# Kernel tuning notes

Hardware: AMD Instinct MI355X
Metric: run time of the kernel (lower is better)

The kernel has to match this reference:

```python
import jax, jax.numpy as jnp
import numpy as np

B, S, E, H, L = 2, 2048, 1024, 16, 64


def setup_inputs() -> dict:
    key = jax.random.key(0)
    ks = jax.random.split(key, 9)
    x = jax.random.normal(ks[0], (B, S, E), dtype=jnp.float32)
    # causal mask: 1 where attention allowed, 0 where blocked (mask==0 -> -inf)
    mask = jnp.tril(jnp.ones((1, S, S), dtype=jnp.int32))
    std = 0.02
    # per-head Linear weights stacked over heads; torch Linear stores W as [out, in]
    Wq = jax.random.normal(ks[1], (H, L, E), dtype=jnp.float32) * std
    Wk = jax.random.normal(ks[2], (H, L, E), dtype=jnp.float32) * std
    Wv = jax.random.normal(ks[3], (H, L, E), dtype=jnp.float32) * std
    bq = jax.random.normal(ks[4], (H, L), dtype=jnp.float32) * std
    bk = jax.random.normal(ks[5], (H, L), dtype=jnp.float32) * std
    bv = jax.random.normal(ks[6], (H, L), dtype=jnp.float32) * std
    Wo = jax.random.normal(ks[7], (E, H * L), dtype=jnp.float32) * std
    bo = jax.random.normal(ks[8], (E,), dtype=jnp.float32) * std
    return {"x": x, "mask": mask, "Wq": Wq, "bq": bq, "Wk": Wk, "bk": bk,
            "Wv": Wv, "bv": bv, "Wo": Wo, "bo": bo}


def reference(x, mask, Wq, bq, Wk, bk, Wv, bv, Wo, bo):
    # Q/K/V for all heads at once: [B, H, S, L]
    Q = jnp.einsum('bse,hle->bhsl', x, Wq) + bq[None, :, None, :]
    K = jnp.einsum('bse,hle->bhsl', x, Wk) + bk[None, :, None, :]
    V = jnp.einsum('bse,hle->bhsl', x, Wv) + bv[None, :, None, :]
    scale = jnp.sqrt(jnp.asarray(L, dtype=Q.dtype))
    scores = jnp.einsum('bhsl,bhtl->bhst', Q, K) / scale  # [B,H,S,S]
    scores = jnp.where(mask[:, None, :, :] == 0, -jnp.inf, scores)
    P = jax.nn.softmax(scores, axis=-1)
    O = jnp.einsum('bhst,bhtl->bhsl', P, V)  # [B,H,S,L]
    # concat heads along last dim (head order matches torch concat)
    z = jnp.transpose(O, (0, 2, 1, 3)).reshape(O.shape[0], O.shape[2], -1)
    return jnp.einsum('bsk,ek->bse', z, Wo) + bo
```

## Files before the change

kernel.cpp:

```cpp
#include <hip/hip_runtime.h>
#include <math.h>

typedef unsigned short US;
typedef __attribute__((ext_vector_type(8))) __bf16 bf16x8;
typedef __attribute__((ext_vector_type(4))) float f32x4;
typedef __attribute__((ext_vector_type(4))) unsigned short us4;

#define MFMA16(a, b, c) __builtin_amdgcn_mfma_f32_16x16x32_bf16(a, b, c, 0, 0, 0)

__device__ __forceinline__ US f2bf(float f) {
  union { float f; unsigned u; } v; v.f = f;
  unsigned r = v.u + 0x7fffu + ((v.u >> 16) & 1u);
  return (US)(r >> 16);
}
__device__ __forceinline__ float bf2f(US u) {
  union { unsigned u; float f; } v; v.u = ((unsigned)u) << 16; return v.f;
}

__device__ __forceinline__ void gload16(const void* g, void* l) {
  __builtin_amdgcn_global_load_lds(
      (const __attribute__((address_space(1))) unsigned int*)g,
      (__attribute__((address_space(3))) unsigned int*)l, 16, 0, 0);
}

__global__ __launch_bounds__(256) void convert_k(
    const float* __restrict__ x, const float* __restrict__ Wq,
    const float* __restrict__ Wk, const float* __restrict__ Wv,
    const float* __restrict__ Wo,
    US* __restrict__ xb, US* __restrict__ wqkv, US* __restrict__ wob) {
  long i = (long)blockIdx.x * blockDim.x + threadIdx.x;
  long e4 = i * 4;
  if (e4 >= 8388608L) return;
  const float* src; US* dst;
  if (e4 < 4194304L) { src = x + e4; dst = xb + e4; }
  else if (e4 < 7340032L) {
    long off = e4 - 4194304L;
    dst = wqkv + off;
    src = (off < 1048576L) ? Wq + off
        : (off < 2097152L ? Wk + (off - 1048576L) : Wv + (off - 2097152L));
  } else {
    long off = e4 - 7340032L;
    src = Wo + off; dst = wob + off;
  }
  float4 v = *(const float4*)src;
  us4 o; o.x = f2bf(v.x); o.y = f2bf(v.y); o.z = f2bf(v.z); o.w = f2bf(v.w);
  *(us4*)dst = o;
}

template <int MODE>
__global__ __launch_bounds__(256) void gemm128(
    const US* __restrict__ A, const US* __restrict__ BT,
    int K, int lda, int ldb, int N,
    const float* __restrict__ b0, const float* __restrict__ b1,
    const float* __restrict__ b2,
    US* __restrict__ oQ, US* __restrict__ oK, US* __restrict__ oV,
    float* __restrict__ oF) {
  __shared__ __align__(16) US As[128 * 32];
  __shared__ __align__(16) US Bs[128 * 32];
  const int tid = threadIdx.x, lane = tid & 63;
  const int w = tid >> 6, wr = w >> 1, wc = w & 1;
  const int m0 = blockIdx.x * 128, n0 = blockIdx.y * 128;
  f32x4 acc[4][4] = {};
  const int r0 = tid >> 2, c0 = (tid & 3) * 8;

  for (int kt = 0; kt < K; kt += 32) {
    gload16(A + (size_t)(m0 + r0) * lda + kt + c0, As + tid * 8);
    gload16(A + (size_t)(m0 + r0 + 64) * lda + kt + c0, As + (tid + 256) * 8);
    gload16(BT + (size_t)(n0 + r0) * ldb + kt + c0, Bs + tid * 8);
    gload16(BT + (size_t)(n0 + r0 + 64) * ldb + kt + c0, Bs + (tid + 256) * 8);
    __syncthreads();
    bf16x8 af[4], bfm[4];
#pragma unroll
    for (int i = 0; i < 4; ++i)
      af[i] = *(const bf16x8*)(As + (wr * 64 + i * 16 + (lane & 15)) * 32 + (lane >> 4) * 8);
#pragma unroll
    for (int j = 0; j < 4; ++j)
      bfm[j] = *(const bf16x8*)(Bs + (wc * 64 + j * 16 + (lane & 15)) * 32 + (lane >> 4) * 8);
#pragma unroll
    for (int i = 0; i < 4; ++i)
#pragma unroll
      for (int j = 0; j < 4; ++j)
        acc[i][j] = MFMA16(af[i], bfm[j], acc[i][j]);
    __syncthreads();
  }

#pragma unroll
  for (int i = 0; i < 4; ++i) {
#pragma unroll
    for (int j = 0; j < 4; ++j) {
#pragma unroll
      for (int r = 0; r < 4; ++r) {
        int m = m0 + wr * 64 + i * 16 + (lane >> 4) * 4 + r;
        int n = n0 + wc * 64 + j * 16 + (lane & 15);
        float v = acc[i][j][r];
        if (MODE == 0) {
          int bb = m >> 11, s = m & 2047;
          int sec = n >> 10, idx = n & 1023;
          int h = idx >> 6, l = idx & 63;
          size_t bhsl = (((size_t)bb * 16 + h) * 2048 + s) * 64 + l;
          if (sec == 0)      oQ[bhsl] = f2bf((v + b0[idx]) * 0.125f);
          else if (sec == 1) oK[bhsl] = f2bf(v + b1[idx]);
          else oV[(((size_t)bb * 16 + h) * 64 + l) * 2048 + s] = f2bf(v + b2[idx]);
        } else {
          oF[(size_t)m * N + n] = v + b0[n];
        }
      }
    }
  }
}

__global__ __launch_bounds__(256) void attn_k(
    const US* __restrict__ Qb, const US* __restrict__ Kb,
    const US* __restrict__ Vtb, US* __restrict__ opart,
    float2* __restrict__ mlpart) {
  __shared__ __align__(16) US Ks[64 * 64];
  __shared__ __align__(16) US Vs[64 * 64];
  __shared__ __align__(16) US Ps[4][16 * 72];
  const int tid = threadIdx.x, lane = tid & 63, w = tid >> 6;
  const int slot = blockIdx.x >> 6;
  const int qt = 31 - slot;
  const int bh = (blockIdx.x & 63) >> 1;
  const int half = blockIdx.x & 1;
  const int h0 = (qt + 2) >> 1;
  const int kstart = half ? h0 : 0;
  const int kend = half ? (qt + 1) : h0;
  const size_t pslot = (size_t)(bh * 32 + qt) * 2 + half;

  if (kstart >= kend) {
    US* op = opart + pslot * 4096;
    us4 z; z.x = 0; z.y = 0; z.z = 0; z.w = 0;
#pragma unroll
    for (int j = 0; j < 4; ++j) *(us4*)(op + tid * 16 + j * 4) = z;
    if ((lane >> 4) == 0)
      mlpart[pslot * 64 + w * 16 + lane] = make_float2(-INFINITY, 0.f);
    return;
  }

  const US* Qp = Qb + ((size_t)bh * 2048 + qt * 64) * 64;
  const char* Kbase = (const char*)(Kb + (size_t)bh * 2048 * 64);
  const char* Vbase = (const char*)(Vtb + (size_t)bh * 64 * 2048);

  const int row0 = tid >> 3, col16 = (tid & 7) * 16;
  const int row1 = row0 + 32;
  const int soff0 = (row0 * 128 + col16) ^ ((row0 & 7) << 4);
  const int soff1 = soff0 + 32 * 128;

  bf16x8 aq[2];
  {
    int qrow = w * 16 + (lane & 15);
#pragma unroll
    for (int kk = 0; kk < 2; ++kk)
      aq[kk] = *(const bf16x8*)(Qp + qrow * 64 + kk * 32 + (lane >> 4) * 8);
  }
  f32x4 o[4] = {};
  float m = -INFINITY, l = 0.f;

  int4 rk0, rk1, rv0, rv1;
#define LOADT(KT)                                                              \
  do {                                                                         \
    rk0 = *(const int4*)(Kbase + ((size_t)((KT)*64 + row0)) * 128 + col16);    \
    rk1 = *(const int4*)(Kbase + ((size_t)((KT)*64 + row1)) * 128 + col16);    \
    rv0 = *(const int4*)(Vbase + (size_t)row0 * 4096 + (KT)*128 + col16);      \
    rv1 = *(const int4*)(Vbase + (size_t)row1 * 4096 + (KT)*128 + col16);      \
  } while (0)
#define WRITET()                                                               \
  do {                                                                         \
    *(int4*)((char*)Ks + soff0) = rk0;                                         \
    *(int4*)((char*)Ks + soff1) = rk1;                                         \
    *(int4*)((char*)Vs + soff0) = rv0;                                         \
    *(int4*)((char*)Vs + soff1) = rv1;                                         \
  } while (0)

  LOADT(kstart);
  WRITET();
  __syncthreads();

  for (int kt = kstart; kt < kend; ++kt) {
    if (kt + 1 < kend) LOADT(kt + 1);

    f32x4 sc[4];
    __builtin_amdgcn_s_setprio(1);
#pragma unroll
    for (int nt = 0; nt < 4; ++nt) {
      f32x4 s = {0.f, 0.f, 0.f, 0.f};
#pragma unroll
      for (int kk = 0; kk < 2; ++kk) {
        int rr = nt * 16 + (lane & 15);
        int off = rr * 128 + kk * 64 + (lane >> 4) * 16;
        off ^= (rr & 7) << 4;
        bf16x8 bkf = *(const bf16x8*)((const char*)Ks + off);
        s = MFMA16(bkf, aq[kk], s);
      }
      sc[nt] = s;
    }
    __builtin_amdgcn_s_setprio(0);

    if (kt == qt) {
      int q_in = w * 16 + (lane & 15);
#pragma unroll
      for (int nt = 0; nt < 4; ++nt)
#pragma unroll
        for (int r = 0; r < 4; ++r) {
          int kv_in = nt * 16 + (lane >> 4) * 4 + r;
          if (kv_in > q_in) sc[nt][r] = -INFINITY;
        }
    }

    {
      float m01 = fmaxf(fmaxf(sc[0][0], sc[0][1]), fmaxf(sc[0][2], sc[0][3]));
      float m23 = fmaxf(fmaxf(sc[1][0], sc[1][1]), fmaxf(sc[1][2], sc[1][3]));
      float m45 = fmaxf(fmaxf(sc[2][0], sc[2][1]), fmaxf(sc[2][2], sc[2][3]));
      float m67 = fmaxf(fmaxf(sc[3][0], sc[3][1]), fmaxf(sc[3][2], sc[3][3]));
      float mx = fmaxf(fmaxf(m01, m23), fmaxf(m45, m67));
      mx = fmaxf(mx, __shfl_xor(mx, 16));
      mx = fmaxf(mx, __shfl_xor(mx, 32));
      float mnew = fmaxf(m, mx);
      float scale = __expf(m - mnew);
      m = mnew;
      float s0 = 0.f, s1 = 0.f, s2 = 0.f, s3 = 0.f;
#pragma unroll
      for (int nt = 0; nt < 4; ++nt) {
        float p0 = __expf(sc[nt][0] - m);
        float p1 = __expf(sc[nt][1] - m);
        float p2 = __expf(sc[nt][2] - m);
        float p3 = __expf(sc[nt][3] - m);
        sc[nt][0] = p0; sc[nt][1] = p1; sc[nt][2] = p2; sc[nt][3] = p3;
        s0 += p0; s1 += p1; s2 += p2; s3 += p3;
      }
      float ssum = (s0 + s1) + (s2 + s3);
      ssum += __shfl_xor(ssum, 16);
      ssum += __shfl_xor(ssum, 32);
      l = l * scale + ssum;
#pragma unroll
      for (int r = 0; r < 4; ++r) {
        float sr = __shfl(scale, ((lane >> 4) << 2) + r, 64);
        o[0][r] *= sr; o[1][r] *= sr; o[2][r] *= sr; o[3][r] *= sr;
      }
    }

    US* pp = &Ps[w][0];
    const int pbase = (lane & 15) * 72 + (lane >> 4) * 4;
#pragma unroll
    for (int nt = 0; nt < 4; ++nt) {
      us4 w4;
      w4.x = f2bf(sc[nt][0]); w4.y = f2bf(sc[nt][1]);
      w4.z = f2bf(sc[nt][2]); w4.w = f2bf(sc[nt][3]);
      *(us4*)(pp + pbase + nt * 16) = w4;
    }

    __builtin_amdgcn_s_setprio(1);
#pragma unroll
    for (int kk = 0; kk < 2; ++kk) {
      bf16x8 pa = *(const bf16x8*)(pp + (lane & 15) * 72 + kk * 32 + (lane >> 4) * 8);
#pragma unroll
      for (int nt = 0; nt < 4; ++nt) {
        int rr = nt * 16 + (lane & 15);
        int off = rr * 128 + kk * 64 + (lane >> 4) * 16;
        off ^= (rr & 7) << 4;
        bf16x8 bvf = *(const bf16x8*)((const char*)Vs + off);
        o[nt] = MFMA16(pa, bvf, o[nt]);
      }
    }
    __builtin_amdgcn_s_setprio(0);

    __syncthreads();
    if (kt + 1 < kend) {
      WRITET();
      __syncthreads();
    }
  }
#undef LOADT
#undef WRITET

  US* op = opart + pslot * 4096;
#pragma unroll
  for (int r = 0; r < 4; ++r) {
    int row = w * 16 + (lane >> 4) * 4 + r;
#pragma unroll
    for (int nt = 0; nt < 4; ++nt) {
      int d = nt * 16 + (lane & 15);
      op[row * 64 + d] = f2bf(o[nt][r]);
    }
  }
  if ((lane >> 4) == 0)
    mlpart[pslot * 64 + w * 16 + lane] = make_float2(m, l);
}

__global__ __launch_bounds__(256) void merge_k(
    const US* __restrict__ opart, const float2* __restrict__ mlpart,
    US* __restrict__ zb) {
  const int t = blockIdx.x;
  const int bh = t >> 5, qt = t & 31;
  const int b = bh >> 4, h = bh & 15;
  const int row = threadIdx.x >> 2;
  const int dg = (threadIdx.x & 3) * 16;
  const US* o1 = opart + ((size_t)t * 2 + 0) * 4096 + row * 64 + dg;
  const US* o2 = opart + ((size_t)t * 2 + 1) * 4096 + row * 64 + dg;
  float2 ml1 = mlpart[(t * 2 + 0) * 64 + row];
  float2 ml2 = mlpart[(t * 2 + 1) * 64 + row];
  float mm = fmaxf(ml1.x, ml2.x);
  float w1 = __expf(ml1.x - mm), w2 = __expf(ml2.x - mm);
  float li = 1.0f / (ml1.y * w1 + ml2.y * w2);
  w1 *= li; w2 *= li;
  int s = qt * 64 + row;
  US* dst = zb + ((size_t)b * 2048 + s) * 1024 + h * 64 + dg;
#pragma unroll
  for (int j = 0; j < 4; ++j) {
    us4 a = *(const us4*)(o1 + j * 4);
    us4 c = *(const us4*)(o2 + j * 4);
    us4 r;
    r.x = f2bf(bf2f(a.x) * w1 + bf2f(c.x) * w2);
    r.y = f2bf(bf2f(a.y) * w1 + bf2f(c.y) * w2);
    r.z = f2bf(bf2f(a.z) * w1 + bf2f(c.z) * w2);
    r.w = f2bf(bf2f(a.w) * w1 + bf2f(c.w) * w2);
    *(us4*)(dst + j * 4) = r;
  }
}

extern "C" void kernel_launch(void* const* d_in, const int* in_sizes, int n_in,
                              void* d_out, int out_size, void* d_ws, size_t ws_size,
                              hipStream_t stream) {
  (void)in_sizes; (void)n_in; (void)out_size; (void)ws_size;
  const float* x  = (const float*)d_in[0];
  const float* Wq = (const float*)d_in[2];
  const float* bq = (const float*)d_in[3];
  const float* Wk = (const float*)d_in[4];
  const float* bk = (const float*)d_in[5];
  const float* Wv = (const float*)d_in[6];
  const float* bv = (const float*)d_in[7];
  const float* Wo = (const float*)d_in[8];
  const float* bo = (const float*)d_in[9];
  char* ws = (char*)d_ws;
  US* xb     = (US*)(ws);
  float2* ml = (float2*)(ws);
  US* zb     = (US*)(ws + 1048576);
  US* wqkv   = (US*)(ws + 8388608);
  US* wob    = (US*)(ws + 14680064);
  US* Qb     = (US*)(ws + 16777216);
  US* Kb     = (US*)(ws + 25165824);
  US* Vtb    = (US*)(ws + 33554432);
  US* opart  = (US*)d_out;
  float* out = (float*)d_out;

  convert_k<<<dim3(8192), dim3(256), 0, stream>>>(x, Wq, Wk, Wv, Wo, xb, wqkv, wob);
  gemm128<0><<<dim3(32, 24), dim3(256), 0, stream>>>(
      xb, wqkv, 1024, 1024, 1024, 3072, bq, bk, bv, Qb, Kb, Vtb, (float*)nullptr);
  attn_k<<<dim3(2048), dim3(256), 0, stream>>>(Qb, Kb, Vtb, opart, ml);
  merge_k<<<dim3(1024), dim3(256), 0, stream>>>(opart, ml, zb);
  gemm128<1><<<dim3(32, 8), dim3(256), 0, stream>>>(
      zb, wob, 1024, 1024, 1024, 1024, bo, (const float*)nullptr, (const float*)nullptr,
      (US*)nullptr, (US*)nullptr, (US*)nullptr, out);
}
```

Before: 140.4 us.

## Deepen GEMM K-step to 64 and switch softmax to exp2 with log2e-folded Q scale

The GEMM kernel now loads two 32-wide K slices per iteration into a doubled shared buffer, which halves the number of barrier pairs per tile. The cost is more LDS per block, which may lower occupancy. Separately, the log2(e) factor is folded into the Q scaling (0.125 becomes 0.18033688), so the attention and merge kernels can use exp2f instead of __expf and skip a multiply per exponential. This keeps the softmax mathematically equivalent up to rounding.

```diff
diff --git a/kernel.cpp b/kernel.cpp
--- a/kernel.cpp
+++ b/kernel.cpp
@@ -55,32 +55,42 @@
     const float* __restrict__ b2,
     US* __restrict__ oQ, US* __restrict__ oK, US* __restrict__ oV,
     float* __restrict__ oF) {
-  __shared__ __align__(16) US As[128 * 32];
-  __shared__ __align__(16) US Bs[128 * 32];
+  __shared__ __align__(16) US As[2][128 * 32];
+  __shared__ __align__(16) US Bs[2][128 * 32];
   const int tid = threadIdx.x, lane = tid & 63;
   const int w = tid >> 6, wr = w >> 1, wc = w & 1;
   const int m0 = blockIdx.x * 128, n0 = blockIdx.y * 128;
   f32x4 acc[4][4] = {};
   const int r0 = tid >> 2, c0 = (tid & 3) * 8;
 
-  for (int kt = 0; kt < K; kt += 32) {
-    gload16(A + (size_t)(m0 + r0) * lda + kt + c0, As + tid * 8);
-    gload16(A + (size_t)(m0 + r0 + 64) * lda + kt + c0, As + (tid + 256) * 8);
-    gload16(BT + (size_t)(n0 + r0) * ldb + kt + c0, Bs + tid * 8);
-    gload16(BT + (size_t)(n0 + r0 + 64) * ldb + kt + c0, Bs + (tid + 256) * 8);
+  for (int kt = 0; kt < K; kt += 64) {
+#pragma unroll
+    for (int h = 0; h < 2; ++h) {
+      gload16(A + (size_t)(m0 + r0) * lda + kt + h * 32 + c0, As[h] + tid * 8);
+      gload16(A + (size_t)(m0 + r0 + 64) * lda + kt + h * 32 + c0,
+              As[h] + (tid + 256) * 8);
+      gload16(BT + (size_t)(n0 + r0) * ldb + kt + h * 32 + c0, Bs[h] + tid * 8);
+      gload16(BT + (size_t)(n0 + r0 + 64) * ldb + kt + h * 32 + c0,
+              Bs[h] + (tid + 256) * 8);
+    }
     __syncthreads();
-    bf16x8 af[4], bfm[4];
-#pragma unroll
-    for (int i = 0; i < 4; ++i)
-      af[i] = *(const bf16x8*)(As + (wr * 64 + i * 16 + (lane & 15)) * 32 + (lane >> 4) * 8);
-#pragma unroll
-    for (int j = 0; j < 4; ++j)
-      bfm[j] = *(const bf16x8*)(Bs + (wc * 64 + j * 16 + (lane & 15)) * 32 + (lane >> 4) * 8);
-#pragma unroll
-    for (int i = 0; i < 4; ++i)
+#pragma unroll
+    for (int h = 0; h < 2; ++h) {
+      bf16x8 af[4], bfm[4];
+#pragma unroll
+      for (int i = 0; i < 4; ++i)
+        af[i] = *(const bf16x8*)(As[h] + (wr * 64 + i * 16 + (lane & 15)) * 32 +
+                                 (lane >> 4) * 8);
 #pragma unroll
       for (int j = 0; j < 4; ++j)
-        acc[i][j] = MFMA16(af[i], bfm[j], acc[i][j]);
+        bfm[j] = *(const bf16x8*)(Bs[h] + (wc * 64 + j * 16 + (lane & 15)) * 32 +
+                                  (lane >> 4) * 8);
+#pragma unroll
+      for (int i = 0; i < 4; ++i)
+#pragma unroll
+        for (int j = 0; j < 4; ++j)
+          acc[i][j] = MFMA16(af[i], bfm[j], acc[i][j]);
+    }
     __syncthreads();
   }
 
@@ -98,7 +108,7 @@
           int sec = n >> 10, idx = n & 1023;
           int h = idx >> 6, l = idx & 63;
           size_t bhsl = (((size_t)bb * 16 + h) * 2048 + s) * 64 + l;
-          if (sec == 0)      oQ[bhsl] = f2bf((v + b0[idx]) * 0.125f);
+          if (sec == 0)      oQ[bhsl] = f2bf((v + b0[idx]) * 0.18033688f);
           else if (sec == 1) oK[bhsl] = f2bf(v + b1[idx]);
           else oV[(((size_t)bb * 16 + h) * 64 + l) * 2048 + s] = f2bf(v + b2[idx]);
         } else {
@@ -215,15 +225,15 @@
       mx = fmaxf(mx, __shfl_xor(mx, 16));
       mx = fmaxf(mx, __shfl_xor(mx, 32));
       float mnew = fmaxf(m, mx);
-      float scale = __expf(m - mnew);
+      float scale = exp2f(m - mnew);
       m = mnew;
       float s0 = 0.f, s1 = 0.f, s2 = 0.f, s3 = 0.f;
 #pragma unroll
       for (int nt = 0; nt < 4; ++nt) {
-        float p0 = __expf(sc[nt][0] - m);
-        float p1 = __expf(sc[nt][1] - m);
-        float p2 = __expf(sc[nt][2] - m);
-        float p3 = __expf(sc[nt][3] - m);
+        float p0 = exp2f(sc[nt][0] - m);
+        float p1 = exp2f(sc[nt][1] - m);
+        float p2 = exp2f(sc[nt][2] - m);
+        float p3 = exp2f(sc[nt][3] - m);
         sc[nt][0] = p0; sc[nt][1] = p1; sc[nt][2] = p2; sc[nt][3] = p3;
         s0 += p0; s1 += p1; s2 += p2; s3 += p3;
       }
@@ -299,7 +309,7 @@
   float2 ml1 = mlpart[(t * 2 + 0) * 64 + row];
   float2 ml2 = mlpart[(t * 2 + 1) * 64 + row];
   float mm = fmaxf(ml1.x, ml2.x);
-  float w1 = __expf(ml1.x - mm), w2 = __expf(ml2.x - mm);
+  float w1 = exp2f(ml1.x - mm), w2 = exp2f(ml2.x - mm);
   float li = 1.0f / (ml1.y * w1 + ml2.y * w2);
   w1 *= li; w2 *= li;
   int s = qt * 64 + row;
```

New measurement: 134.3 us. -4.3%, faster.
